# Kernel optimization log

Hardware: AMD Instinct MI355X
Metric: run time of the kernel (lower is better)

The kernel has to match this reference:

```python
import jax, jax.numpy as jnp
import numpy as np


def setup_inputs() -> dict:
    key = jax.random.key(0)
    k1, k2 = jax.random.split(key)
    emb_in = jax.random.normal(k1, (2048, 32), dtype=jnp.float32)
    sum_weights = jax.random.normal(k2, (2048,), dtype=jnp.float32)
    return {"emb_in": emb_in, "sum_weights": sum_weights}


def reference(emb_in, sum_weights):
    # emb_in: [n, f], sum_weights: [n]
    n, f = emb_in.shape
    # a[k] = emb_in[k // n]  (each row repeated n times consecutively)
    a = jnp.repeat(emb_in, n, axis=0)          # [n*n, f]
    # b[k] = emb_in[k % n]   (whole tensor tiled n times)
    b = jnp.tile(emb_in, (n, 1))               # [n*n, f]
    # weights column matches b: w[k] = sum_weights[k % n]
    w = jnp.tile(sum_weights[:, None], (n, 1)) # [n*n, 1]
    sample = jnp.concatenate((a, b, w), axis=1)  # [n*n, 2*f + 1]
    return sample
```

## Files before the change

### kernel.cpp

```cpp
#include <hip/hip_runtime.h>


#define NROWS 2048u
#define ICHUNK 16u
#define JSLAB 16u
#define SLAB_FLOATS (JSLAB * 65u)
#define SLAB_F4 (SLAB_FLOATS / 4u)
#define ROW_F4 (NROWS * 65u / 4u)

typedef float f32x4 __attribute__((ext_vector_type(4)));

__global__ __launch_bounds__(256) void expand_reuse(
    const float* __restrict__ emb,
    const float* __restrict__ sw,
    f32x4* __restrict__ out)
{
    __shared__ __align__(16) float lds[4][SLAB_FLOATS];

    const unsigned tid  = threadIdx.x;
    const unsigned wave = tid >> 6;
    const unsigned lane = tid & 63u;

    const unsigned bi = blockIdx.x >> 5;
    const unsigned bj = blockIdx.x & 31u;
    const unsigned i0 = bi * ICHUNK;
    const unsigned j0 = bj * 64u + wave * JSLAB;

    float* W = &lds[wave][0];

    {
        const f32x4* ej = (const f32x4*)(emb + (size_t)j0 * 32u);
        const f32x4 b0 = ej[lane];
        const f32x4 b1 = ej[lane + 64u];
        const unsigned d0 = (lane >> 3) * 65u + 32u + (lane & 7u) * 4u;
        W[d0 + 0u] = b0.x; W[d0 + 1u] = b0.y;
        W[d0 + 2u] = b0.z; W[d0 + 3u] = b0.w;
        W[d0 + 520u + 0u] = b1.x; W[d0 + 520u + 1u] = b1.y;
        W[d0 + 520u + 2u] = b1.z; W[d0 + 520u + 3u] = b1.w;
        if (lane < JSLAB) W[lane * 65u + 64u] = sw[j0 + lane];
    }

    float va[ICHUNK];
#pragma unroll
    for (unsigned k = 0; k < ICHUNK; ++k)
        va[k] = emb[(i0 + k) * 32u + (lane & 31u)];

    const unsigned rbase = (lane >> 5) * 8u;
    const unsigned c     = lane & 31u;

    unsigned ob = i0 * ROW_F4 + ((j0 * 65u) >> 2);

    const f32x4* L4 = (const f32x4*)W;

#pragma unroll
    for (unsigned k = 0; k < ICHUNK; ++k) {
#pragma unroll
        for (unsigned rp = 0; rp < 8u; ++rp)
            W[(rbase + rp) * 65u + c] = va[k];

#pragma unroll
        for (unsigned p = 0; p < 4u; ++p)
            __builtin_nontemporal_store(L4[p * 64u + lane],
                                        &out[ob + p * 64u + lane]);
        if (lane < 4u)
            __builtin_nontemporal_store(L4[256u + lane],
                                        &out[ob + 256u + lane]);

        ob += ROW_F4;
    }
}

extern "C" void kernel_launch(void* const* d_in, const int* in_sizes, int n_in,
                              void* d_out, int out_size, void* d_ws, size_t ws_size,
                              hipStream_t stream) {
    const float* emb = (const float*)d_in[0];
    const float* sw  = (const float*)d_in[1];
    f32x4* out       = (f32x4*)d_out;

    const unsigned blocks = (NROWS / ICHUNK) * (NROWS / 64u);
    expand_reuse<<<dim3(blocks), dim3(256), 0, stream>>>(emb, sw, out);
}
```

Measured before the change: 227.5 us.

## Switch to persistent grid-stride slab sweep with double-buffered LDS images

Replaces the 4096-block launch with 256 persistent blocks. Each wave sweeps output slabs in a grid-stride pattern so that, at each step, all waves write a contiguous region of the output. Two LDS images are double-buffered so the next slab's 'a' columns are filled while the current one is stored, and the emb reads for upcoming slabs are prefetched into registers. Stores also change from nontemporal to normal, which may change cache behaviour on this purely write-bound kernel.

```diff
diff --git a/kernel.cpp b/kernel.cpp
--- a/kernel.cpp
+++ b/kernel.cpp
@@ -2,71 +2,89 @@
 
 
 #define NROWS 2048u
-#define ICHUNK 16u
-#define JSLAB 16u
-#define SLAB_FLOATS (JSLAB * 65u)
+#define SLAB_ROWS 16u
+#define SLAB_FLOATS (SLAB_ROWS * 65u)
 #define SLAB_F4 (SLAB_FLOATS / 4u)
-#define ROW_F4 (NROWS * 65u / 4u)
+#define NBLOCKS 256u
+#define NWAVES (NBLOCKS * 4u)
+#define TOTAL_SLABS (NROWS * NROWS / SLAB_ROWS)
+#define ITERS (TOTAL_SLABS / NWAVES)
 
 typedef float f32x4 __attribute__((ext_vector_type(4)));
 
-__global__ __launch_bounds__(256) void expand_reuse(
+__global__ __launch_bounds__(256) void expand_sweep(
     const float* __restrict__ emb,
     const float* __restrict__ sw,
     f32x4* __restrict__ out)
 {
-    __shared__ __align__(16) float lds[4][SLAB_FLOATS];
+    __shared__ __align__(16) float lds[4][2][SLAB_FLOATS];
 
-    const unsigned tid  = threadIdx.x;
-    const unsigned wave = tid >> 6;
-    const unsigned lane = tid & 63u;
+    const unsigned tid   = threadIdx.x;
+    const unsigned wave  = tid >> 6;
+    const unsigned lane  = tid & 63u;
+    const unsigned W     = blockIdx.x * 4u + wave;
+    const unsigned j0    = (W & 127u) * SLAB_ROWS;
+    const unsigned ibase = W >> 7;
+    const unsigned c     = lane & 31u;
+    const unsigned rbase = (lane >> 5) * 8u;
 
-    const unsigned bi = blockIdx.x >> 5;
-    const unsigned bj = blockIdx.x & 31u;
-    const unsigned i0 = bi * ICHUNK;
-    const unsigned j0 = bj * 64u + wave * JSLAB;
-
-    float* W = &lds[wave][0];
+    float* img0 = &lds[wave][0][0];
+    float* img1 = &lds[wave][1][0];
 
     {
         const f32x4* ej = (const f32x4*)(emb + (size_t)j0 * 32u);
         const f32x4 b0 = ej[lane];
         const f32x4 b1 = ej[lane + 64u];
         const unsigned d0 = (lane >> 3) * 65u + 32u + (lane & 7u) * 4u;
-        W[d0 + 0u] = b0.x; W[d0 + 1u] = b0.y;
-        W[d0 + 2u] = b0.z; W[d0 + 3u] = b0.w;
-        W[d0 + 520u + 0u] = b1.x; W[d0 + 520u + 1u] = b1.y;
-        W[d0 + 520u + 2u] = b1.z; W[d0 + 520u + 3u] = b1.w;
-        if (lane < JSLAB) W[lane * 65u + 64u] = sw[j0 + lane];
+        img0[d0 + 0u] = b0.x; img0[d0 + 1u] = b0.y;
+        img0[d0 + 2u] = b0.z; img0[d0 + 3u] = b0.w;
+        img0[d0 + 520u] = b1.x; img0[d0 + 521u] = b1.y;
+        img0[d0 + 522u] = b1.z; img0[d0 + 523u] = b1.w;
+        img1[d0 + 0u] = b0.x; img1[d0 + 1u] = b0.y;
+        img1[d0 + 2u] = b0.z; img1[d0 + 3u] = b0.w;
+        img1[d0 + 520u] = b1.x; img1[d0 + 521u] = b1.y;
+        img1[d0 + 522u] = b1.z; img1[d0 + 523u] = b1.w;
+        if (lane < SLAB_ROWS) {
+            const float s0 = sw[j0 + lane];
+            img0[lane * 65u + 64u] = s0;
+            img1[lane * 65u + 64u] = s0;
+        }
     }
 
-    float va[ICHUNK];
-#pragma unroll
-    for (unsigned k = 0; k < ICHUNK; ++k)
-        va[k] = emb[(i0 + k) * 32u + (lane & 31u)];
-
-    const unsigned rbase = (lane >> 5) * 8u;
-    const unsigned c     = lane & 31u;
-
-    unsigned ob = i0 * ROW_F4 + ((j0 * 65u) >> 2);
-
-    const f32x4* L4 = (const f32x4*)W;
-
-#pragma unroll
-    for (unsigned k = 0; k < ICHUNK; ++k) {
+    float va1, va2;
+    {
+        const float va0 = emb[ibase * 32u + c];
 #pragma unroll
         for (unsigned rp = 0; rp < 8u; ++rp)
-            W[(rbase + rp) * 65u + c] = va[k];
+            img0[(rbase + rp) * 65u + c] = va0;
+        va1 = emb[(ibase + 8u) * 32u + c];
+        va2 = emb[(ibase + 16u) * 32u + c];
+    }
 
+    unsigned slab = W;
+#pragma unroll 2
+    for (unsigned t = 0; t < ITERS; ++t) {
+        float* CUR = (t & 1u) ? img1 : img0;
+        float* NXT = (t & 1u) ? img0 : img1;
+
+        const f32x4* L4 = (const f32x4*)CUR;
+        const unsigned ob = slab * SLAB_F4;
 #pragma unroll
         for (unsigned p = 0; p < 4u; ++p)
-            __builtin_nontemporal_store(L4[p * 64u + lane],
-                                        &out[ob + p * 64u + lane]);
+            out[ob + p * 64u + lane] = L4[p * 64u + lane];
         if (lane < 4u)
-            __builtin_nontemporal_store(L4[256u + lane],
-                                        &out[ob + 256u + lane]);
+            out[ob + 256u + lane] = L4[256u + lane];
 
-        ob += ROW_F4;
+        if (t + 1u < ITERS) {
+#pragma unroll
+            for (unsigned rp = 0; rp < 8u; ++rp)
+                NXT[(rbase + rp) * 65u + c] = va1;
+        }
+        va1 = va2;
+        if (t + 3u < ITERS)
+            va2 = emb[(ibase + (t + 3u) * 8u) * 32u + c];
+
+        slab += NWAVES;
     }
 }
 
@@ -77,6 +95,5 @@
     const float* sw  = (const float*)d_in[1];
     f32x4* out       = (f32x4*)d_out;
 
-    const unsigned blocks = (NROWS / ICHUNK) * (NROWS / 64u);
-    expand_reuse<<<dim3(blocks), dim3(256), 0, stream>>>(emb, sw, out);
+    expand_sweep<<<dim3(NBLOCKS), dim3(256), 0, stream>>>(emb, sw, out);
 }
```

After: 233.8 us. 2.7% more time.
